# Kernel optimization log

Measured on AMD Instinct MI355X. Metric: run time of the kernel, lower is better.

## Reference

```python
import jax, jax.numpy as jnp
import numpy as np

N_NODES = 100000
N_EDGES = 1600000
N_FEAT, N_HID, N_CLS = 256, 64, 16


def setup_inputs() -> dict:
    key = jax.random.key(0)
    ks = jax.random.split(key, 8)
    x = jax.random.normal(ks[0], (N_NODES, N_FEAT), dtype=jnp.float32)
    adj_row = jax.random.randint(ks[1], (N_EDGES,), 0, N_NODES, dtype=jnp.int32)
    adj_col = jax.random.randint(ks[2], (N_EDGES,), 0, N_NODES, dtype=jnp.int32)
    adj_vals = jax.random.uniform(ks[3], (N_EDGES,), dtype=jnp.float32)
    W1 = jax.random.normal(ks[4], (N_FEAT, N_HID), dtype=jnp.float32) * 0.05
    b1 = jnp.zeros((N_HID,), dtype=jnp.float32)
    W2 = jax.random.normal(ks[5], (N_HID, N_CLS), dtype=jnp.float32) * 0.05
    b2 = jnp.zeros((N_CLS,), dtype=jnp.float32)
    return {"x": x, "adj_row": adj_row, "adj_col": adj_col, "adj_vals": adj_vals,
            "W1": W1, "b1": b1, "W2": W2, "b2": b2}


def _spmm(row, col, vals, h):
    # sparse [N,N] @ dense [N,D]: gather source rows, scale, scatter-add to dest rows
    msgs = vals[:, None] * h[col]                       # [E, D]
    return jax.ops.segment_sum(msgs, row, num_segments=N_NODES)


def reference(x, adj_row, adj_col, adj_vals, W1, b1, W2, b2):
    # layer 1: linear -> spmm -> relu  (dropout is identity at inference)
    h = _spmm(adj_row, adj_col, adj_vals, x @ W1 + b1)  # [N, n_hidden]
    h = jax.nn.relu(h)
    # layer 2: linear -> spmm -> log_softmax
    out = _spmm(adj_row, adj_col, adj_vals, h @ W2 + b2)  # [N, n_class]
    return jax.nn.log_softmax(out, axis=1)
```

## Files before the change

### kernel.cpp

```cpp
#include <hip/hip_runtime.h>

#define N_NODES 100000
#define N_EDGES 1600000
#define N_FEAT  256
#define N_HID   64
#define N_CLS   16
#define NB      391
#define CHUNK   8192

typedef unsigned short bfraw;
typedef unsigned int uint32;

typedef __attribute__((ext_vector_type(8))) short  bf16x8;
typedef __attribute__((ext_vector_type(4))) float  f32x4;

__device__ __forceinline__ bfraw f2bf(float f) {
    union { float f; unsigned int i; } v; v.f = f;
    unsigned int x = v.i;
    return (bfraw)((x + 0x7FFFu + ((x >> 16) & 1u)) >> 16);
}

__device__ __forceinline__ float bf_lo(uint32 g) { return __uint_as_float(g << 16); }
__device__ __forceinline__ float bf_hi(uint32 g) { return __uint_as_float(g & 0xFFFF0000u); }

__global__ __launch_bounds__(256) void w1cvt_hist_k(const float* __restrict__ W1,
                                                    bfraw* __restrict__ w1f,
                                                    const int* __restrict__ rowi,
                                                    int* __restrict__ bcnt) {
    __shared__ int lh[NB];
    if (blockIdx.x < 64) {
        int i = blockIdx.x * 256 + threadIdx.x;
        int k = i >> 6, n = i & 63;
        w1f[((size_t)((k >> 3) * 64 + n) << 3) + (k & 7)] = f2bf(W1[i]);
        return;
    }
    for (int i = threadIdx.x; i < NB; i += 256) lh[i] = 0;
    __syncthreads();
    for (int e = (blockIdx.x - 64) * 256 + threadIdx.x; e < N_EDGES; e += 256 * 256)
        atomicAdd(&lh[rowi[e] >> 8], 1);
    __syncthreads();
    for (int i = threadIdx.x; i < NB; i += 256) {
        int c = lh[i];
        if (c) atomicAdd(&bcnt[i], c);
    }
}

__global__ __launch_bounds__(256) void gemm1_k(const float* __restrict__ x,
                                               const bfraw* __restrict__ w1f,
                                               const float* __restrict__ b1,
                                               bfraw* __restrict__ h0) {
    const int t    = threadIdx.x;
    const int w    = t >> 6;
    const int lane = t & 63;
    const int q    = lane >> 4;
    const int m    = lane & 15;

    const int row  = blockIdx.x * 64 + w * 16 + m;
    const int srow = row < N_NODES ? row : N_NODES - 1;
    const float* xp = x + (size_t)srow * N_FEAT + q * 8;
    const bf16x8* w1v = (const bf16x8*)w1f;

    f32x4 acc[4];
    #pragma unroll
    for (int nt = 0; nt < 4; ++nt) acc[nt] = (f32x4){0.f, 0.f, 0.f, 0.f};

    #pragma unroll
    for (int s = 0; s < 8; ++s) {
        float4 a0 = *(const float4*)(xp + s * 32);
        float4 a1 = *(const float4*)(xp + s * 32 + 4);
        bf16x8 af;
        af[0] = (short)f2bf(a0.x); af[1] = (short)f2bf(a0.y);
        af[2] = (short)f2bf(a0.z); af[3] = (short)f2bf(a0.w);
        af[4] = (short)f2bf(a1.x); af[5] = (short)f2bf(a1.y);
        af[6] = (short)f2bf(a1.z); af[7] = (short)f2bf(a1.w);
        const int g = s * 4 + q;
        #pragma unroll
        for (int nt = 0; nt < 4; ++nt) {
            bf16x8 bf_ = w1v[g * 64 + nt * 16 + m];
            acc[nt] = __builtin_amdgcn_mfma_f32_16x16x32_bf16(af, bf_, acc[nt], 0, 0, 0);
        }
    }

    float bb[4];
    #pragma unroll
    for (int nt = 0; nt < 4; ++nt) bb[nt] = b1[nt * 16 + m];

    const int orow0 = blockIdx.x * 64 + w * 16 + q * 4;
    #pragma unroll
    for (int r = 0; r < 4; ++r) {
        int orow = orow0 + r;
        if (orow < N_NODES) {
            bfraw* op = h0 + (size_t)orow * N_HID + m;
            #pragma unroll
            for (int nt = 0; nt < 4; ++nt)
                op[nt * 16] = f2bf(acc[nt][r] + bb[nt]);
        }
    }
}

__global__ __launch_bounds__(512) void bscan_k(const int* __restrict__ bcnt,
                                               int* __restrict__ bbase,
                                               int* __restrict__ gcur,
                                               int* __restrict__ rp) {
    __shared__ int s[512];
    int t = threadIdx.x;
    int v = (t < NB) ? bcnt[t] : 0;
    s[t] = v;
    __syncthreads();
    #pragma unroll
    for (int off = 1; off < 512; off <<= 1) {
        int x = (t >= off) ? s[t - off] : 0;
        __syncthreads();
        s[t] += x;
        __syncthreads();
    }
    if (t <= NB) {
        int b = s[t] - v;
        bbase[t] = b;
        if (t < NB) gcur[t] = b;
    }
    if (t == 0) rp[N_NODES] = N_EDGES;
}

__global__ __launch_bounds__(256) void scatter_k(const int* __restrict__ rowi,
                                                 const int* __restrict__ coli,
                                                 const float* __restrict__ vals,
                                                 int* __restrict__ gcur,
                                                 int2* __restrict__ edges) {
    __shared__ int lh[NB];
    __shared__ int lb[NB];
    const int t  = threadIdx.x;
    const int e0 = blockIdx.x * CHUNK;
    for (int i = t; i < NB; i += 256) lh[i] = 0;
    __syncthreads();
    for (int j = t; j < CHUNK; j += 256) {
        int e = e0 + j;
        if (e < N_EDGES) atomicAdd(&lh[rowi[e] >> 8], 1);
    }
    __syncthreads();
    for (int i = t; i < NB; i += 256) {
        int c = lh[i];
        lb[i] = c ? atomicAdd(&gcur[i], c) : 0;
        lh[i] = 0;
    }
    __syncthreads();
    for (int j = t; j < CHUNK; j += 256) {
        int e = e0 + j;
        if (e < N_EDGES) {
            int r  = rowi[e];
            int b  = r >> 8;
            int rk = atomicAdd(&lh[b], 1);
            edges[lb[b] + rk] = make_int2(coli[e] | ((r & 255) << 17),
                                          __float_as_int(vals[e]));
        }
    }
}

__global__ __launch_bounds__(256) void sort_k(const int* __restrict__ bbase,
                                              const int2* __restrict__ edges,
                                              int2* __restrict__ edges2,
                                              int* __restrict__ rp) {
    __shared__ int cnt[256];
    __shared__ int pos[256];
    const int t   = threadIdx.x;
    const int b   = blockIdx.x;
    const int beg = bbase[b];
    const int end = bbase[b + 1];

    cnt[t] = 0;
    __syncthreads();
    for (int i = beg + t; i < end; i += 256)
        atomicAdd(&cnt[(edges[i].x >> 17) & 255], 1);
    __syncthreads();

    int v = cnt[t];
    pos[t] = v;
    __syncthreads();
    #pragma unroll
    for (int off = 1; off < 256; off <<= 1) {
        int y = (t >= off) ? pos[t - off] : 0;
        __syncthreads();
        pos[t] += y;
        __syncthreads();
    }
    int excl = pos[t] - v;

    int row = (b << 8) + t;
    if (row < N_NODES) rp[row] = beg + excl;
    __syncthreads();
    pos[t] = excl;
    __syncthreads();

    for (int i = beg + t; i < end; i += 256) {
        int2 E = edges[i];
        int r  = (E.x >> 17) & 255;
        int rk = atomicAdd(&pos[r], 1);
        edges2[beg + rk] = make_int2(E.x & 0x1FFFF, E.y);
    }
}

__global__ __launch_bounds__(256) void spmm1_fused3_k(const int* __restrict__ rp,
                                                      const int2* __restrict__ edges2,
                                                      const uint32* __restrict__ h0p,
                                                      const float* __restrict__ W2,
                                                      const float* __restrict__ b2,
                                                      float* __restrict__ h2) {
    __shared__ float Hs[16][68];
    __shared__ float Ws[64 * 16];
    __shared__ float bs[16];
    const int t = threadIdx.x;
    *(float4*)&Ws[t * 4] = ((const float4*)W2)[t];
    if (t < 16) bs[t] = b2[t];

    const int g16 = t >> 4;
    const int l   = t & 15;
    const int row = blockIdx.x * 16 + g16;
    const int beg = rp[row];
    const int end = rp[row + 1];

    const uint2* h0v = (const uint2*)h0p;

    float a0 = 0.f, a1 = 0.f, a2 = 0.f, a3 = 0.f;
    int i = beg;
    for (; i + 4 <= end; i += 4) {
        int2 E0 = edges2[i + 0];
        int2 E1 = edges2[i + 1];
        int2 E2 = edges2[i + 2];
        int2 E3 = edges2[i + 3];
        uint2 q0 = h0v[(size_t)E0.x * 16 + l];
        uint2 q1 = h0v[(size_t)E1.x * 16 + l];
        uint2 q2 = h0v[(size_t)E2.x * 16 + l];
        uint2 q3 = h0v[(size_t)E3.x * 16 + l];
        float v0 = __int_as_float(E0.y);
        float v1 = __int_as_float(E1.y);
        float v2 = __int_as_float(E2.y);
        float v3 = __int_as_float(E3.y);
        a0 += v0 * bf_lo(q0.x); a1 += v0 * bf_hi(q0.x);
        a2 += v0 * bf_lo(q0.y); a3 += v0 * bf_hi(q0.y);
        a0 += v1 * bf_lo(q1.x); a1 += v1 * bf_hi(q1.x);
        a2 += v1 * bf_lo(q1.y); a3 += v1 * bf_hi(q1.y);
        a0 += v2 * bf_lo(q2.x); a1 += v2 * bf_hi(q2.x);
        a2 += v2 * bf_lo(q2.y); a3 += v2 * bf_hi(q2.y);
        a0 += v3 * bf_lo(q3.x); a1 += v3 * bf_hi(q3.x);
        a2 += v3 * bf_lo(q3.y); a3 += v3 * bf_hi(q3.y);
    }
    for (; i < end; ++i) {
        int2 E = edges2[i];
        uint2 q = h0v[(size_t)E.x * 16 + l];
        float v = __int_as_float(E.y);
        a0 += v * bf_lo(q.x); a1 += v * bf_hi(q.x);
        a2 += v * bf_lo(q.y); a3 += v * bf_hi(q.y);
    }

    *(float4*)&Hs[g16][4 * l] = make_float4(fmaxf(a0, 0.f), fmaxf(a1, 0.f),
                                            fmaxf(a2, 0.f), fmaxf(a3, 0.f));
    __syncthreads();

    const int r = t >> 4;
    const int c = t & 15;
    float a = bs[c];
    #pragma unroll
    for (int k = 0; k < 64; ++k)
        a += Hs[r][k] * Ws[k * 16 + c];
    h2[(size_t)(blockIdx.x * 16 + r) * N_CLS + c] = a;
}

__global__ __launch_bounds__(256) void spmm2_lsm_k(const int* __restrict__ rp,
                                                   const int2* __restrict__ edges2,
                                                   const float* __restrict__ h2,
                                                   float* __restrict__ outp) {
    const int lane = threadIdx.x & 15;
    const int row  = blockIdx.x * 16 + (threadIdx.x >> 4);
    const int beg = rp[row];
    const int end = rp[row + 1];
    float acc = 0.f;
    int i = beg;
    for (; i + 4 <= end; i += 4) {
        int2 e0 = edges2[i + 0], e1 = edges2[i + 1];
        int2 e2 = edges2[i + 2], e3 = edges2[i + 3];
        float g0 = h2[(size_t)e0.x * N_CLS + lane];
        float g1 = h2[(size_t)e1.x * N_CLS + lane];
        float g2 = h2[(size_t)e2.x * N_CLS + lane];
        float g3 = h2[(size_t)e3.x * N_CLS + lane];
        acc += __int_as_float(e0.y) * g0;
        acc += __int_as_float(e1.y) * g1;
        acc += __int_as_float(e2.y) * g2;
        acc += __int_as_float(e3.y) * g3;
    }
    for (; i < end; ++i) {
        int2 e = edges2[i];
        acc += __int_as_float(e.y) * h2[(size_t)e.x * N_CLS + lane];
    }

    float m = acc;
    #pragma unroll
    for (int off = 8; off; off >>= 1) m = fmaxf(m, __shfl_xor(m, off, 16));
    float ex = expf(acc - m);
    float s = ex;
    #pragma unroll
    for (int off = 8; off; off >>= 1) s += __shfl_xor(s, off, 16);
    outp[(size_t)row * N_CLS + lane] = acc - m - logf(s);
}

extern "C" void kernel_launch(void* const* d_in, const int* in_sizes, int n_in,
                              void* d_out, int out_size, void* d_ws, size_t ws_size,
                              hipStream_t stream) {
    const float* x        = (const float*)d_in[0];
    const int*   adj_row  = (const int*)d_in[1];
    const int*   adj_col  = (const int*)d_in[2];
    const float* adj_vals = (const float*)d_in[3];
    const float* W1       = (const float*)d_in[4];
    const float* b1       = (const float*)d_in[5];
    const float* W2       = (const float*)d_in[6];
    const float* b2       = (const float*)d_in[7];
    float*       out      = (float*)d_out;

    const size_t H0_BYTES = (size_t)N_NODES * N_HID * sizeof(bfraw);
    const size_t H2_BYTES = (size_t)N_NODES * N_CLS * sizeof(float);
    const size_t E_BYTES  = (size_t)N_EDGES * sizeof(int2);
    bfraw* h0     = (bfraw*)d_ws;
    float* h2     = (float*)((char*)d_ws + H0_BYTES);
    int2*  edges  = (int2*)((char*)h2 + H2_BYTES);
    int2*  edges2 = (int2*)((char*)edges + E_BYTES);
    int*   bcnt   = (int*)((char*)edges2 + E_BYTES);
    int*   bbase  = bcnt + NB;
    int*   gcur   = bbase + NB + 1;
    int*   rp     = gcur + NB;
    bfraw* w1f    = (bfraw*)(rp + N_NODES + 1);

    hipMemsetAsync(bcnt, 0, NB * sizeof(int), stream);
    w1cvt_hist_k<<<320, 256, 0, stream>>>(W1, w1f, adj_row, bcnt);
    bscan_k<<<1, 512, 0, stream>>>(bcnt, bbase, gcur, rp);
    scatter_k<<<(N_EDGES + CHUNK - 1) / CHUNK, 256, 0, stream>>>(adj_row, adj_col,
                                                                 adj_vals, gcur, edges);
    sort_k<<<NB, 256, 0, stream>>>(bbase, edges, edges2, rp);

    gemm1_k<<<(N_NODES + 63) / 64, 256, 0, stream>>>(x, w1f, b1, h0);
    spmm1_fused3_k<<<N_NODES / 16, 256, 0, stream>>>(rp, edges2, (const uint32*)h0,
                                                     W2, b2, h2);

    spmm2_lsm_k<<<N_NODES / 16, 256, 0, stream>>>(rp, edges2, h2, out);
}
```

Before: 338.3 us.

## Build CSR with per-row atomic histogram, single-block scan, and direct atomic scatter

Replaces the two-level bucket sort (bucket histogram, bucket scan, bucket scatter, per-bucket local sort) with a per-row global atomic histogram, a single-block 1024-thread prefix scan over all rows, and a direct atomic scatter into the final edge array. This removes one full pass over the edges and the intermediate edge buffer. In exchange it uses global atomics per edge for both counting and placement, and a serial single-block scan. Edge order within a row becomes nondeterministic, which can change floating-point summation order.

```diff
diff --git a/kernel.cpp b/kernel.cpp
--- a/kernel.cpp
+++ b/kernel.cpp
@@ -5,8 +5,6 @@
 #define N_FEAT  256
 #define N_HID   64
 #define N_CLS   16
-#define NB      391
-#define CHUNK   8192
 
 typedef unsigned short bfraw;
 typedef unsigned int uint32;
@@ -23,25 +21,78 @@
 __device__ __forceinline__ float bf_lo(uint32 g) { return __uint_as_float(g << 16); }
 __device__ __forceinline__ float bf_hi(uint32 g) { return __uint_as_float(g & 0xFFFF0000u); }
 
-__global__ __launch_bounds__(256) void w1cvt_hist_k(const float* __restrict__ W1,
-                                                    bfraw* __restrict__ w1f,
-                                                    const int* __restrict__ rowi,
-                                                    int* __restrict__ bcnt) {
-    __shared__ int lh[NB];
+__global__ __launch_bounds__(256) void w1cvt_rowhist_k(const float* __restrict__ W1,
+                                                       bfraw* __restrict__ w1f,
+                                                       const int* __restrict__ rowi,
+                                                       int* __restrict__ rcnt) {
     if (blockIdx.x < 64) {
         int i = blockIdx.x * 256 + threadIdx.x;
         int k = i >> 6, n = i & 63;
         w1f[((size_t)((k >> 3) * 64 + n) << 3) + (k & 7)] = f2bf(W1[i]);
         return;
     }
-    for (int i = threadIdx.x; i < NB; i += 256) lh[i] = 0;
-    __syncthreads();
     for (int e = (blockIdx.x - 64) * 256 + threadIdx.x; e < N_EDGES; e += 256 * 256)
-        atomicAdd(&lh[rowi[e] >> 8], 1);
-    __syncthreads();
-    for (int i = threadIdx.x; i < NB; i += 256) {
-        int c = lh[i];
-        if (c) atomicAdd(&bcnt[i], c);
+        atomicAdd(&rcnt[rowi[e]], 1);
+}
+
+__global__ __launch_bounds__(1024) void scan_k(const int* __restrict__ rcnt,
+                                               int* __restrict__ rp,
+                                               int* __restrict__ gcur) {
+    __shared__ int wsum[16];
+    const int t  = threadIdx.x;
+    const int wv = t >> 6;
+    const int ln = t & 63;
+    int carry = 0;
+    for (int tile = 0; tile < 25; ++tile) {
+        int base = tile * 4096 + t * 4;
+        int4 v;
+        if (base + 4 <= N_NODES) {
+            v = *(const int4*)(rcnt + base);
+        } else {
+            v.x = (base + 0 < N_NODES) ? rcnt[base + 0] : 0;
+            v.y = (base + 1 < N_NODES) ? rcnt[base + 1] : 0;
+            v.z = (base + 2 < N_NODES) ? rcnt[base + 2] : 0;
+            v.w = (base + 3 < N_NODES) ? rcnt[base + 3] : 0;
+        }
+        const int tot = v.x + v.y + v.z + v.w;
+        int inc = tot;
+        #pragma unroll
+        for (int off = 1; off < 64; off <<= 1) {
+            int y = __shfl_up(inc, off);
+            if (ln >= off) inc += y;
+        }
+        if (ln == 63) wsum[wv] = inc;
+        __syncthreads();
+        if (t < 16) {
+            int x = wsum[t];
+            #pragma unroll
+            for (int off = 1; off < 16; off <<= 1) {
+                int y = __shfl_up(x, off, 16);
+                if (t >= off) x += y;
+            }
+            wsum[t] = x;
+        }
+        __syncthreads();
+        int excl = carry + (wv ? wsum[wv - 1] : 0) + (inc - tot);
+        if (base + 0 < N_NODES) { rp[base + 0] = excl; gcur[base + 0] = excl; }
+        if (base + 1 < N_NODES) { int e1 = excl + v.x;             rp[base + 1] = e1; gcur[base + 1] = e1; }
+        if (base + 2 < N_NODES) { int e2 = excl + v.x + v.y;       rp[base + 2] = e2; gcur[base + 2] = e2; }
+        if (base + 3 < N_NODES) { int e3 = excl + v.x + v.y + v.z; rp[base + 3] = e3; gcur[base + 3] = e3; }
+        carry += wsum[15];
+        __syncthreads();
+    }
+    if (t == 0) rp[N_NODES] = N_EDGES;
+}
+
+__global__ __launch_bounds__(256) void scatter2_k(const int* __restrict__ rowi,
+                                                  const int* __restrict__ coli,
+                                                  const float* __restrict__ vals,
+                                                  int* __restrict__ gcur,
+                                                  int2* __restrict__ edges2) {
+    for (int e = blockIdx.x * 256 + threadIdx.x; e < N_EDGES; e += gridDim.x * 256) {
+        int r   = rowi[e];
+        int pos = atomicAdd(&gcur[r], 1);
+        edges2[pos] = make_int2(coli[e], __float_as_int(vals[e]));
     }
 }
 
@@ -95,107 +146,6 @@
             for (int nt = 0; nt < 4; ++nt)
                 op[nt * 16] = f2bf(acc[nt][r] + bb[nt]);
         }
-    }
-}
-
-__global__ __launch_bounds__(512) void bscan_k(const int* __restrict__ bcnt,
-                                               int* __restrict__ bbase,
-                                               int* __restrict__ gcur,
-                                               int* __restrict__ rp) {
-    __shared__ int s[512];
-    int t = threadIdx.x;
-    int v = (t < NB) ? bcnt[t] : 0;
-    s[t] = v;
-    __syncthreads();
-    #pragma unroll
-    for (int off = 1; off < 512; off <<= 1) {
-        int x = (t >= off) ? s[t - off] : 0;
-        __syncthreads();
-        s[t] += x;
-        __syncthreads();
-    }
-    if (t <= NB) {
-        int b = s[t] - v;
-        bbase[t] = b;
-        if (t < NB) gcur[t] = b;
-    }
-    if (t == 0) rp[N_NODES] = N_EDGES;
-}
-
-__global__ __launch_bounds__(256) void scatter_k(const int* __restrict__ rowi,
-                                                 const int* __restrict__ coli,
-                                                 const float* __restrict__ vals,
-                                                 int* __restrict__ gcur,
-                                                 int2* __restrict__ edges) {
-    __shared__ int lh[NB];
-    __shared__ int lb[NB];
-    const int t  = threadIdx.x;
-    const int e0 = blockIdx.x * CHUNK;
-    for (int i = t; i < NB; i += 256) lh[i] = 0;
-    __syncthreads();
-    for (int j = t; j < CHUNK; j += 256) {
-        int e = e0 + j;
-        if (e < N_EDGES) atomicAdd(&lh[rowi[e] >> 8], 1);
-    }
-    __syncthreads();
-    for (int i = t; i < NB; i += 256) {
-        int c = lh[i];
-        lb[i] = c ? atomicAdd(&gcur[i], c) : 0;
-        lh[i] = 0;
-    }
-    __syncthreads();
-    for (int j = t; j < CHUNK; j += 256) {
-        int e = e0 + j;
-        if (e < N_EDGES) {
-            int r  = rowi[e];
-            int b  = r >> 8;
-            int rk = atomicAdd(&lh[b], 1);
-            edges[lb[b] + rk] = make_int2(coli[e] | ((r & 255) << 17),
-                                          __float_as_int(vals[e]));
-        }
-    }
-}
-
-__global__ __launch_bounds__(256) void sort_k(const int* __restrict__ bbase,
-                                              const int2* __restrict__ edges,
-                                              int2* __restrict__ edges2,
-                                              int* __restrict__ rp) {
-    __shared__ int cnt[256];
-    __shared__ int pos[256];
-    const int t   = threadIdx.x;
-    const int b   = blockIdx.x;
-    const int beg = bbase[b];
-    const int end = bbase[b + 1];
-
-    cnt[t] = 0;
-    __syncthreads();
-    for (int i = beg + t; i < end; i += 256)
-        atomicAdd(&cnt[(edges[i].x >> 17) & 255], 1);
-    __syncthreads();
-
-    int v = cnt[t];
-    pos[t] = v;
-    __syncthreads();
-    #pragma unroll
-    for (int off = 1; off < 256; off <<= 1) {
-        int y = (t >= off) ? pos[t - off] : 0;
-        __syncthreads();
-        pos[t] += y;
-        __syncthreads();
-    }
-    int excl = pos[t] - v;
-
-    int row = (b << 8) + t;
-    if (row < N_NODES) rp[row] = beg + excl;
-    __syncthreads();
-    pos[t] = excl;
-    __syncthreads();
-
-    for (int i = beg + t; i < end; i += 256) {
-        int2 E = edges[i];
-        int r  = (E.x >> 17) & 255;
-        int rk = atomicAdd(&pos[r], 1);
-        edges2[beg + rk] = make_int2(E.x & 0x1FFFF, E.y);
     }
 }
 
@@ -315,25 +265,22 @@
     const float* b2       = (const float*)d_in[7];
     float*       out      = (float*)d_out;
 
-    const size_t H0_BYTES = (size_t)N_NODES * N_HID * sizeof(bfraw);
-    const size_t H2_BYTES = (size_t)N_NODES * N_CLS * sizeof(float);
-    const size_t E_BYTES  = (size_t)N_EDGES * sizeof(int2);
+    const size_t H0_BYTES  = (size_t)N_NODES * N_HID * sizeof(bfraw);
+    const size_t H2_BYTES  = (size_t)N_NODES * N_CLS * sizeof(float);
+    const size_t E_BYTES   = (size_t)N_EDGES * sizeof(int2);
+    const size_t W1F_BYTES = (size_t)N_FEAT * N_HID * sizeof(bfraw);
     bfraw* h0     = (bfraw*)d_ws;
     float* h2     = (float*)((char*)d_ws + H0_BYTES);
-    int2*  edges  = (int2*)((char*)h2 + H2_BYTES);
-    int2*  edges2 = (int2*)((char*)edges + E_BYTES);
-    int*   bcnt   = (int*)((char*)edges2 + E_BYTES);
-    int*   bbase  = bcnt + NB;
-    int*   gcur   = bbase + NB + 1;
-    int*   rp     = gcur + NB;
-    bfraw* w1f    = (bfraw*)(rp + N_NODES + 1);
-
-    hipMemsetAsync(bcnt, 0, NB * sizeof(int), stream);
-    w1cvt_hist_k<<<320, 256, 0, stream>>>(W1, w1f, adj_row, bcnt);
-    bscan_k<<<1, 512, 0, stream>>>(bcnt, bbase, gcur, rp);
-    scatter_k<<<(N_EDGES + CHUNK - 1) / CHUNK, 256, 0, stream>>>(adj_row, adj_col,
-                                                                 adj_vals, gcur, edges);
-    sort_k<<<NB, 256, 0, stream>>>(bbase, edges, edges2, rp);
+    int2*  edges2 = (int2*)((char*)h2 + H2_BYTES);
+    bfraw* w1f    = (bfraw*)((char*)edges2 + E_BYTES);
+    int*   rcnt   = (int*)((char*)w1f + W1F_BYTES);
+    int*   rp     = rcnt + N_NODES;
+    int*   gcur   = rp + N_NODES + 1;
+
+    hipMemsetAsync(rcnt, 0, N_NODES * sizeof(int), stream);
+    w1cvt_rowhist_k<<<320, 256, 0, stream>>>(W1, w1f, adj_row, rcnt);
+    scan_k<<<1, 1024, 0, stream>>>(rcnt, rp, gcur);
+    scatter2_k<<<1024, 256, 0, stream>>>(adj_row, adj_col, adj_vals, gcur, edges2);
 
     gemm1_k<<<(N_NODES + 63) / 64, 256, 0, stream>>>(x, w1f, b1, h0);
     spmm1_fused3_k<<<N_NODES / 16, 256, 0, stream>>>(rp, edges2, (const uint32*)h0,
```

After: 475.6 us. 1.41x slower.
